# Optimization experiments

Hardware: AMD Instinct MI355X
Metric: run time of the kernel (lower is better)

The kernel has to match this reference:

```python
import jax, jax.numpy as jnp
import numpy as np

START_TIME = 10
CODING_TIME = 10
REMAIN_TIME = 5
V_TH = 1.0

# surrogate-gradient spike: forward is Heaviside(x>0)
@jax.custom_vjp
def spike(x):
    return (x > 0).astype(x.dtype)

def _spike_fwd(x):
    return spike(x), x

def _spike_bwd(x, g):
    lens = 0.5
    gamma = 0.5
    temp = jnp.exp(-x * x / (2.0 * lens * lens)) / jnp.sqrt(2.0 * jnp.pi) / lens
    return (g * temp * gamma,)

spike.defvjp(_spike_fwd, _spike_bwd)

B, T, I, H, O = 500, 100, 700, 512, 20

def setup_inputs() -> dict:
    key = jax.random.key(0)
    ks = jax.random.split(key, 9)
    half = I // 2
    input_data = jax.random.normal(ks[0], (B, T, I), dtype=jnp.float32)
    target = jax.random.randint(ks[1], (B, T), 0, O, dtype=jnp.int32).astype(jnp.int64)
    v_init = jax.random.uniform(ks[2], (B, H), dtype=jnp.float32)  # torch.rand init
    lim = 1.0 / np.sqrt(half)
    W1 = jax.random.uniform(ks[3], (H, half), minval=-lim, maxval=lim, dtype=jnp.float32)
    W2 = jax.random.uniform(ks[4], (H, half), minval=-lim, maxval=lim, dtype=jnp.float32)
    tau_n = jax.random.uniform(ks[5], (2, H), minval=2.0, maxval=6.0, dtype=jnp.float32)
    tau_m = jax.random.uniform(ks[6], (H,), minval=0.0, maxval=4.0, dtype=jnp.float32)
    lim_o = 1.0 / np.sqrt(H)
    Wout = jax.random.uniform(ks[7], (O, H), minval=-lim_o, maxval=lim_o, dtype=jnp.float32)
    bout = jax.random.uniform(ks[8], (O,), minval=-lim_o, maxval=lim_o, dtype=jnp.float32)
    return {"input_data": input_data, "target": target, "v_init": v_init,
            "W1": W1, "W2": W2, "tau_n": tau_n, "tau_m": tau_m,
            "Wout": Wout, "bout": bout}

def reference(input_data, target, v_init, W1, W2, tau_n, tau_m, Wout, bout):
    Bs, Ts, Is = input_data.shape
    half = Is // 2
    # precompute both branch drives for all timesteps: [T, B, H]
    b1 = jnp.einsum('bti,hi->tbh', input_data[:, :, :half], W1)
    b2 = jnp.einsum('bti,hi->tbh', input_data[:, :, half:], W2)
    beta1 = jax.nn.sigmoid(tau_n[0])  # [H]
    beta2 = jax.nn.sigmoid(tau_n[1])  # [H]
    alpha = jax.nn.sigmoid(tau_m)     # [H]

    def step(carry, inp):
        d1, d2, v, s = carry
        x1, x2 = inp
        d1 = beta1 * d1 + (1.0 - beta1) * x1
        d2 = beta2 * d2 + (1.0 - beta2) * x2
        v = alpha * v + (1.0 - alpha) * (d1 + d2) - V_TH * s
        s = spike(v - V_TH)
        return (d1, d2, v, s), s

    z = jnp.zeros_like(v_init)
    (_, _, _, _), spikes = jax.lax.scan(step, (z, z, v_init, z), (b1, b2))  # spikes: [T,B,H]
    output_history = jnp.einsum('tbh,oh->bto', spikes, Wout) + bout  # [B,T,O]

    ts = np.arange(Ts)
    mask_np = ((ts - START_TIME) % (CODING_TIME + REMAIN_TIME) > REMAIN_TIME) & (ts > START_TIME)
    mask = jnp.asarray(mask_np, dtype=output_history.dtype)  # [T]

    # faithful double-softmax: CrossEntropyLoss applied to softmax(output)
    p = jax.nn.softmax(output_history, axis=-1)
    logp = jax.nn.log_softmax(p, axis=-1)
    tgt = target.astype(jnp.int32)
    ce = -jnp.take_along_axis(logp, tgt[..., None], axis=-1)[..., 0]  # [B,T]
    loss_per_t = ce.mean(axis=0)  # mean over batch, per timestep
    total_loss = jnp.sum(loss_per_t * mask)

    pred = jnp.argmax(p, axis=-1)  # [B,T]
    total_correct = jnp.sum((pred == tgt).astype(jnp.int32) * mask_np[None, :].astype(np.int32))
    total_samples = int(mask_np.sum()) * Bs
    return total_loss, output_history, total_correct, total_samples
```

## Files before the change

kernel.cpp:

```cpp
#include <hip/hip_runtime.h>
#include <hip/hip_bf16.h>
#include <math.h>

#define B_    500
#define T_    100
#define I_    700
#define HALF_ 350
#define H_    512
#define O_    20
#define M_    (B_*T_)
#define BH_   (B_*H_)
#define TP_   112
#define KP_   352
#define ASTR_ 40
#define ABUF_ (TP_*ASTR_)
#define DRB_  116
#define NB_   12500

#define START_T  10
#define CODING_T 10
#define REMAIN_T 5

typedef __attribute__((ext_vector_type(8))) short short8v;
typedef __attribute__((ext_vector_type(8))) unsigned short ushort8v;
typedef __attribute__((ext_vector_type(4))) float f32x4;
typedef __attribute__((ext_vector_type(2))) float f32x2;

__device__ __forceinline__ float sigmoidf_(float x) {
  return 1.0f / (1.0f + expf(-x));
}

__device__ __forceinline__ unsigned cvtpk(float lo, float hi) {
  unsigned r;
  asm("v_cvt_pk_bf16_f32 %0, %1, %2" : "=v"(r) : "v"(lo), "v"(hi));
  return r;
}

__device__ __forceinline__ unsigned cvtpk_fp8x4(float f0, float f1, float f2, float f3) {
  int r = __builtin_amdgcn_cvt_pk_fp8_f32(f0, f1, 0, false);
  r = __builtin_amdgcn_cvt_pk_fp8_f32(f2, f3, r, true);
  return (unsigned)r;
}

__device__ __forceinline__ unsigned short f2bf(float f) {
  unsigned u = __float_as_uint(f);
  u = (u + 0x7fffu + ((u >> 16) & 1u)) >> 16;
  return (unsigned short)u;
}

__global__ __launch_bounds__(256) void convert_w(
    const float* __restrict__ W1, const float* __restrict__ W2,
    unsigned short* __restrict__ wb)
{
  const int idx = blockIdx.x * 256 + threadIdx.x;
  const int ph  = idx / (H_ * (KP_ / 8));
  const int rem = idx % (H_ * (KP_ / 8));
  const int h   = rem / (KP_ / 8);
  const int cc  = (rem % (KP_ / 8)) * 8;
  ushort8v v;
#pragma unroll
  for (int j = 0; j < 8; ++j) {
    const int kk = cc + j;
    float f;
    if (ph == 0) f = (kk < HALF_) ? W1[(size_t)h * HALF_ + kk] : 0.0f;
    else         f = (kk >= 2)    ? W2[(size_t)h * HALF_ + kk - 2] : 0.0f;
    v[j] = f2bf(f);
  }
  *reinterpret_cast<ushort8v*>(wb + (((size_t)ph * H_ + h) * KP_) + cc) = v;
}

__global__ __launch_bounds__(1024, 4) void fused_drive_scan(
    const float* __restrict__ input, const unsigned short* __restrict__ Wb,
    const float* __restrict__ v_init, const float* __restrict__ tau_n,
    const float* __restrict__ tau_m, unsigned char* __restrict__ spikes)
{
  __shared__ __align__(16) unsigned short As[2 * ABUF_];
  __shared__ __align__(4) unsigned char d1c[H_ * DRB_];
  __shared__ __align__(4) unsigned char d2c[H_ * DRB_];

  const int tid  = threadIdx.x;
  const int lane = tid & 63;
  const int w    = tid >> 6;
  const int b    = blockIdx.x;

  const int sr = tid >> 3;
  const int so = (tid & 7) * 4;
  const bool stLd = (tid < 800);
  const bool stZr = (tid >= 800) && (tid < 896);
  const float* aBase = input + ((size_t)b * T_ + (stLd ? sr : 0)) * I_ + so;
  unsigned short* aDst = As + sr * ASTR_ + so;

  const int brow = w * 32 + (lane & 15);
  const int kcS  = (lane >> 4) * 8;
  const unsigned short* bBase0 = Wb + (size_t)brow * KP_ + kcS;
  const unsigned short* bBase1 = Wb + (size_t)(brow + 16) * KP_ + kcS;
  const int arow = lane & 15;

  f32x4 acc[7][2];
#pragma unroll
  for (int i = 0; i < 7; ++i) {
    acc[i][0] = f32x4{0.f, 0.f, 0.f, 0.f};
    acc[i][1] = f32x4{0.f, 0.f, 0.f, 0.f};
  }

  float4 aR;
  short8v bC0, bC1, bN0, bN1;

  if (stZr) {
    const uint2 z = {0, 0};
    *(uint2*)(aDst) = z;
    *(uint2*)(aDst + ABUF_) = z;
  }
  if (stLd) aR = *(const float4*)(aBase);
  bC0 = *reinterpret_cast<const short8v*>(bBase0);
  bC1 = *reinterpret_cast<const short8v*>(bBase1);
  bN0 = *reinterpret_cast<const short8v*>(bBase0 + 32);
  bN1 = *reinterpret_cast<const short8v*>(bBase1 + 32);
  if (stLd) {
    const uint2 p = {cvtpk(aR.x, aR.y), cvtpk(aR.z, aR.w)};
    *(uint2*)(aDst) = p;
    aR = *(const float4*)(aBase + 32);
  }
  asm volatile("s_waitcnt lgkmcnt(0)" ::: "memory");
  __builtin_amdgcn_s_barrier();
  asm volatile("" ::: "memory");

#pragma unroll 1
  for (int k = 0; k < 22; ++k) {
    const int buf  = (k & 1) * ABUF_;
    const int nbuf = ((k + 1) & 1) * ABUF_;
    short8v a[7];
#pragma unroll
    for (int i = 0; i < 7; ++i)
      a[i] = *reinterpret_cast<const short8v*>(As + buf + (arow + i * 16) * ASTR_ + kcS);
#pragma unroll
    for (int i = 0; i < 7; ++i) {
      acc[i][0] = __builtin_amdgcn_mfma_f32_16x16x32_bf16(a[i], bC0, acc[i][0], 0, 0, 0);
      acc[i][1] = __builtin_amdgcn_mfma_f32_16x16x32_bf16(a[i], bC1, acc[i][1], 0, 0, 0);
    }
    bC0 = bN0; bC1 = bN1;
    if (k < 21 && stLd) {
      const uint2 p = {cvtpk(aR.x, aR.y), cvtpk(aR.z, aR.w)};
      *(uint2*)(aDst + nbuf) = p;
    }
    if (k < 20 && stLd) {
      const int kn  = k + 2;
      const int ph  = (kn >= 11);
      const int k0  = (kn - ph * 11) * 32;
      aR = *(const float4*)(aBase + (ph ? 348 : 0) + k0);
    }
    if (k < 20) {
      const int kb  = k + 2;
      const int phb = (kb >= 11);
      const size_t bo = (size_t)phb * H_ * KP_ + (kb - phb * 11) * 32;
      bN0 = *reinterpret_cast<const short8v*>(bBase0 + bo);
      bN1 = *reinterpret_cast<const short8v*>(bBase1 + bo);
    }
    if (k == 10 || k == 21) {
      unsigned char* ds = (k == 10) ? d1c : d2c;
#pragma unroll
      for (int i = 0; i < 7; ++i) {
        const int tb = i * 16 + ((lane >> 4) << 2);
#pragma unroll
        for (int j = 0; j < 2; ++j) {
          const int hl = w * 32 + j * 16 + (lane & 15);
          const unsigned r =
              cvtpk_fp8x4(acc[i][j][0], acc[i][j][1], acc[i][j][2], acc[i][j][3]);
          *(unsigned*)(ds + hl * DRB_ + tb) = r;
          acc[i][j] = f32x4{0.f, 0.f, 0.f, 0.f};
        }
      }
    }
    asm volatile("s_waitcnt lgkmcnt(0)" ::: "memory");
    __builtin_amdgcn_s_barrier();
    asm volatile("" ::: "memory");
  }

  if (tid < H_) {
    const int hg = tid;
    const float beta1 = sigmoidf_(tau_n[hg]);
    const float beta2 = sigmoidf_(tau_n[H_ + hg]);
    const float alpha = sigmoidf_(tau_m[hg]);
    const float ob1 = 1.0f - beta1, ob2 = 1.0f - beta2, oa = 1.0f - alpha;

    float d1 = 0.0f, d2 = 0.0f, s = 0.0f;
    float v = v_init[(size_t)b * H_ + hg];
    const unsigned char* r1 = d1c + hg * DRB_;
    const unsigned char* r2 = d2c + hg * DRB_;
    unsigned char* sp = spikes + (size_t)b * H_ + hg;
#pragma unroll 1
    for (int c = 0; c < 25; ++c) {
      const unsigned u1 = *(const unsigned*)(r1 + c * 4);
      const unsigned u2 = *(const unsigned*)(r2 + c * 4);
      const f32x2 a1 = __builtin_amdgcn_cvt_pk_f32_fp8((int)u1, false);
      const f32x2 b1 = __builtin_amdgcn_cvt_pk_f32_fp8((int)u1, true);
      const f32x2 a2 = __builtin_amdgcn_cvt_pk_f32_fp8((int)u2, false);
      const f32x2 b2 = __builtin_amdgcn_cvt_pk_f32_fp8((int)u2, true);
      const float f1[4] = {a1[0], a1[1], b1[0], b1[1]};
      const float f2[4] = {a2[0], a2[1], b2[0], b2[1]};
#pragma unroll
      for (int j = 0; j < 4; ++j) {
        d1 = beta1 * d1 + ob1 * f1[j];
        d2 = beta2 * d2 + ob2 * f2[j];
        v = alpha * v + oa * (d1 + d2) - s;
        s = (v > 1.0f) ? 1.0f : 0.0f;
        sp[(size_t)(c * 4 + j) * BH_] = (unsigned char)s;
      }
    }
  }
}

__global__ __launch_bounds__(256) void out_loss(
    const unsigned char* __restrict__ spikes, const float* __restrict__ Wout,
    const float* __restrict__ bout, const int* __restrict__ target,
    float* __restrict__ oh, float* __restrict__ partials)
{
  const int lane = threadIdx.x & 63;
  const int widx = threadIdx.x >> 6;
  const int bt = blockIdx.x * 4 + widx;
  const int b = bt / T_, t = bt - b * T_;

  const unsigned char* srow = spikes + ((size_t)t * B_ + b) * H_;
  const uint2 sv = *(const uint2*)(srow + lane * 8);

  float acc[O_];
#pragma unroll
  for (int o = 0; o < O_; ++o) acc[o] = 0.0f;

#pragma unroll
  for (int j = 0; j < 8; ++j) {
    const unsigned sb = ((j < 4) ? (sv.x >> (8 * j)) : (sv.y >> (8 * (j - 4)))) & 255u;
    if (sb) {
      const int hh = lane * 8 + j;
#pragma unroll
      for (int o = 0; o < O_; ++o) acc[o] += Wout[o * H_ + hh];
    }
  }
#pragma unroll
  for (int o = 0; o < O_; ++o) {
#pragma unroll
    for (int off = 32; off > 0; off >>= 1) acc[o] += __shfl_down(acc[o], off);
  }

  __shared__ float sl[4], sc[4];
  if (lane == 0) {
    float r[O_];
    float* orow = oh + ((size_t)b * T_ + t) * O_;
#pragma unroll
    for (int o = 0; o < O_; ++o) { r[o] = acc[o] + bout[o]; orow[o] = r[o]; }

    float lossc = 0.0f, corr = 0.0f;
    const bool maskv = (t > START_T) && (((t - START_T) % (CODING_T + REMAIN_T)) > REMAIN_T);
    if (maskv) {
      float m = r[0];
#pragma unroll
      for (int o = 1; o < O_; ++o) m = fmaxf(m, r[o]);
      const int tgt = target[(size_t)b * T_ + t];
      float e[O_], S = 0.0f, etgt = 0.0f;
#pragma unroll
      for (int o = 0; o < O_; ++o) {
        e[o] = expf(r[o] - m);
        S += e[o];
        etgt = (o == tgt) ? e[o] : etgt;
      }
      const float inv = 1.0f / S;
      const float pm = inv;
      float S2 = 0.0f;
#pragma unroll
      for (int o = 0; o < O_; ++o) S2 += expf(e[o] * inv - pm);
      const float lse = pm + logf(S2);
      lossc = (lse - etgt * inv) * (1.0f / (float)B_);
      int pred = 0;
      float bm = r[0];
#pragma unroll
      for (int o = 1; o < O_; ++o) { if (r[o] > bm) { bm = r[o]; pred = o; } }
      corr = (pred == tgt) ? 1.0f : 0.0f;
    }
    sl[widx] = lossc; sc[widx] = corr;
  }
  __syncthreads();
  if (threadIdx.x == 0) {
    partials[blockIdx.x]       = sl[0] + sl[1] + sl[2] + sl[3];
    partials[NB_ + blockIdx.x] = sc[0] + sc[1] + sc[2] + sc[3];
  }
}

__global__ __launch_bounds__(256) void loss_final(
    const float* __restrict__ partials, float* __restrict__ out, float samples)
{
  float a = 0.0f, c = 0.0f;
  for (int i = threadIdx.x; i < NB_; i += 256) { a += partials[i]; c += partials[NB_ + i]; }
  __shared__ float sl[256], sc[256];
  sl[threadIdx.x] = a; sc[threadIdx.x] = c;
  __syncthreads();
  for (int s = 128; s > 0; s >>= 1) {
    if (threadIdx.x < s) {
      sl[threadIdx.x] += sl[threadIdx.x + s];
      sc[threadIdx.x] += sc[threadIdx.x + s];
    }
    __syncthreads();
  }
  if (threadIdx.x == 0) {
    out[0] = sl[0];
    out[1 + (size_t)M_ * O_] = sc[0];
    out[2 + (size_t)M_ * O_] = samples;
  }
}

extern "C" void kernel_launch(void* const* d_in, const int* in_sizes, int n_in,
                              void* d_out, int out_size, void* d_ws, size_t ws_size,
                              hipStream_t stream) {
  const float* input  = (const float*)d_in[0];
  const int*   target = (const int*)d_in[1];
  const float* v_init = (const float*)d_in[2];
  const float* W1     = (const float*)d_in[3];
  const float* W2     = (const float*)d_in[4];
  const float* tau_n  = (const float*)d_in[5];
  const float* tau_m  = (const float*)d_in[6];
  const float* Wout   = (const float*)d_in[7];
  const float* bout   = (const float*)d_in[8];
  float* out = (float*)d_out;
  float* oh  = out + 1;

  unsigned short* Wb = (unsigned short*)d_ws;
  unsigned char* spikes = (unsigned char*)(Wb + (size_t)2 * H_ * KP_);
  float* partials = (float*)(spikes + (size_t)T_ * BH_);

  hipLaunchKernelGGL(convert_w, dim3((2 * H_ * KP_ / 8) / 256), dim3(256), 0, stream,
                     W1, W2, Wb);

  hipLaunchKernelGGL(fused_drive_scan, dim3(B_), dim3(1024), 0, stream,
                     input, Wb, v_init, tau_n, tau_m, spikes);

  hipLaunchKernelGGL(out_loss, dim3(NB_), dim3(256), 0, stream,
                     spikes, Wout, bout, target, oh, partials);

  int mcount = 0;
  for (int t = 0; t < T_; ++t)
    if (t > START_T && ((t - START_T) % (CODING_T + REMAIN_T)) > REMAIN_T) mcount++;
  hipLaunchKernelGGL(loss_final, dim3(1), dim3(256), 0, stream, partials,
                     out, (float)(mcount * B_));
}
```

Measured before the change: 164.9 us.

## Fuse output projection and loss into scan kernel using LDS spike bitmasks

The separate out_loss kernel is removed. Spikes are packed into per-neuron 32-bit bitmasks in shared memory (reusing the A buffer) instead of being written as bytes to global memory. Each of the 16 wavefronts then computes output logits, softmax loss and accuracy for its timesteps and reduces to one partial per batch row. This drops the 25.6 MB spike round trip and a kernel launch. In exchange the scan block does the output work serially per block, and the loss_final reduction shrinks to 500 partials.

```diff
diff --git a/kernel.cpp b/kernel.cpp
--- a/kernel.cpp
+++ b/kernel.cpp
@@ -15,7 +15,6 @@
 #define ASTR_ 40
 #define ABUF_ (TP_*ASTR_)
 #define DRB_  116
-#define NB_   12500
 
 #define START_T  10
 #define CODING_T 10
@@ -69,14 +68,17 @@
   *reinterpret_cast<ushort8v*>(wb + (((size_t)ph * H_ + h) * KP_) + cc) = v;
 }
 
-__global__ __launch_bounds__(1024, 4) void fused_drive_scan(
+__global__ __launch_bounds__(1024, 4) void fused_all(
     const float* __restrict__ input, const unsigned short* __restrict__ Wb,
     const float* __restrict__ v_init, const float* __restrict__ tau_n,
-    const float* __restrict__ tau_m, unsigned char* __restrict__ spikes)
+    const float* __restrict__ tau_m, const float* __restrict__ Wout,
+    const float* __restrict__ bout, const int* __restrict__ target,
+    float* __restrict__ oh, float* __restrict__ partials)
 {
   __shared__ __align__(16) unsigned short As[2 * ABUF_];
   __shared__ __align__(4) unsigned char d1c[H_ * DRB_];
   __shared__ __align__(4) unsigned char d2c[H_ * DRB_];
+  __shared__ float redL[16], redC[16];
 
   const int tid  = threadIdx.x;
   const int lane = tid & 63;
@@ -176,6 +178,7 @@
     asm volatile("" ::: "memory");
   }
 
+  unsigned* sbits = (unsigned*)As;
   if (tid < H_) {
     const int hg = tid;
     const float beta1 = sigmoidf_(tau_n[hg]);
@@ -187,69 +190,76 @@
     float v = v_init[(size_t)b * H_ + hg];
     const unsigned char* r1 = d1c + hg * DRB_;
     const unsigned char* r2 = d2c + hg * DRB_;
-    unsigned char* sp = spikes + (size_t)b * H_ + hg;
+#pragma unroll
+    for (int wi = 0; wi < 4; ++wi) {
+      unsigned bits = 0;
+#pragma unroll
+      for (int cc = 0; cc < 8; ++cc) {
+        if (wi == 3 && cc >= 1) break;
+        const int c = wi * 8 + cc;
+        const unsigned u1 = *(const unsigned*)(r1 + c * 4);
+        const unsigned u2 = *(const unsigned*)(r2 + c * 4);
+        const f32x2 a1 = __builtin_amdgcn_cvt_pk_f32_fp8((int)u1, false);
+        const f32x2 b1 = __builtin_amdgcn_cvt_pk_f32_fp8((int)u1, true);
+        const f32x2 a2 = __builtin_amdgcn_cvt_pk_f32_fp8((int)u2, false);
+        const f32x2 b2 = __builtin_amdgcn_cvt_pk_f32_fp8((int)u2, true);
+        const float f1[4] = {a1[0], a1[1], b1[0], b1[1]};
+        const float f2[4] = {a2[0], a2[1], b2[0], b2[1]};
+#pragma unroll
+        for (int j = 0; j < 4; ++j) {
+          d1 = beta1 * d1 + ob1 * f1[j];
+          d2 = beta2 * d2 + ob2 * f2[j];
+          v = alpha * v + oa * (d1 + d2) - s;
+          const bool spk = (v > 1.0f);
+          s = spk ? 1.0f : 0.0f;
+          bits |= ((unsigned)spk) << (cc * 4 + j);
+        }
+      }
+      sbits[wi * H_ + hg] = bits;
+    }
+  }
+  __syncthreads();
+
+  float bo[O_];
+#pragma unroll
+  for (int o = 0; o < O_; ++o) bo[o] = bout[o];
+
+  float lossAcc = 0.0f, corrAcc = 0.0f;
+  const int hbase = lane * 8;
 #pragma unroll 1
-    for (int c = 0; c < 25; ++c) {
-      const unsigned u1 = *(const unsigned*)(r1 + c * 4);
-      const unsigned u2 = *(const unsigned*)(r2 + c * 4);
-      const f32x2 a1 = __builtin_amdgcn_cvt_pk_f32_fp8((int)u1, false);
-      const f32x2 b1 = __builtin_amdgcn_cvt_pk_f32_fp8((int)u1, true);
-      const f32x2 a2 = __builtin_amdgcn_cvt_pk_f32_fp8((int)u2, false);
-      const f32x2 b2 = __builtin_amdgcn_cvt_pk_f32_fp8((int)u2, true);
-      const float f1[4] = {a1[0], a1[1], b1[0], b1[1]};
-      const float f2[4] = {a2[0], a2[1], b2[0], b2[1]};
-#pragma unroll
-      for (int j = 0; j < 4; ++j) {
-        d1 = beta1 * d1 + ob1 * f1[j];
-        d2 = beta2 * d2 + ob2 * f2[j];
-        v = alpha * v + oa * (d1 + d2) - s;
-        s = (v > 1.0f) ? 1.0f : 0.0f;
-        sp[(size_t)(c * 4 + j) * BH_] = (unsigned char)s;
+  for (int t = w; t < T_; t += 16) {
+    const unsigned* sb = sbits + (t >> 5) * H_ + hbase;
+    const uint4 wa = *(const uint4*)(sb);
+    const uint4 wb2 = *(const uint4*)(sb + 4);
+    const unsigned sel = t & 31;
+    const unsigned wv[8] = {wa.x, wa.y, wa.z, wa.w, wb2.x, wb2.y, wb2.z, wb2.w};
+
+    float acco[O_];
+#pragma unroll
+    for (int o = 0; o < O_; ++o) acco[o] = 0.0f;
+#pragma unroll
+    for (int j = 0; j < 8; ++j) {
+      if ((wv[j] >> sel) & 1u) {
+        const int hh = hbase + j;
+#pragma unroll
+        for (int o = 0; o < O_; ++o) acco[o] += Wout[o * H_ + hh];
       }
     }
-  }
-}
-
-__global__ __launch_bounds__(256) void out_loss(
-    const unsigned char* __restrict__ spikes, const float* __restrict__ Wout,
-    const float* __restrict__ bout, const int* __restrict__ target,
-    float* __restrict__ oh, float* __restrict__ partials)
-{
-  const int lane = threadIdx.x & 63;
-  const int widx = threadIdx.x >> 6;
-  const int bt = blockIdx.x * 4 + widx;
-  const int b = bt / T_, t = bt - b * T_;
-
-  const unsigned char* srow = spikes + ((size_t)t * B_ + b) * H_;
-  const uint2 sv = *(const uint2*)(srow + lane * 8);
-
-  float acc[O_];
-#pragma unroll
-  for (int o = 0; o < O_; ++o) acc[o] = 0.0f;
-
-#pragma unroll
-  for (int j = 0; j < 8; ++j) {
-    const unsigned sb = ((j < 4) ? (sv.x >> (8 * j)) : (sv.y >> (8 * (j - 4)))) & 255u;
-    if (sb) {
-      const int hh = lane * 8 + j;
-#pragma unroll
-      for (int o = 0; o < O_; ++o) acc[o] += Wout[o * H_ + hh];
-    }
-  }
-#pragma unroll
-  for (int o = 0; o < O_; ++o) {
-#pragma unroll
-    for (int off = 32; off > 0; off >>= 1) acc[o] += __shfl_down(acc[o], off);
-  }
-
-  __shared__ float sl[4], sc[4];
-  if (lane == 0) {
+#pragma unroll
+    for (int o = 0; o < O_; ++o) {
+#pragma unroll
+      for (int off = 32; off; off >>= 1) acco[o] += __shfl_xor(acco[o], off);
+    }
     float r[O_];
-    float* orow = oh + ((size_t)b * T_ + t) * O_;
-#pragma unroll
-    for (int o = 0; o < O_; ++o) { r[o] = acc[o] + bout[o]; orow[o] = r[o]; }
-
-    float lossc = 0.0f, corr = 0.0f;
+#pragma unroll
+    for (int o = 0; o < O_; ++o) r[o] = acco[o] + bo[o];
+
+    if (lane == 0) {
+      float* orow = oh + ((size_t)b * T_ + t) * O_;
+#pragma unroll
+      for (int o = 0; o < O_; ++o) orow[o] = r[o];
+    }
+
     const bool maskv = (t > START_T) && (((t - START_T) % (CODING_T + REMAIN_T)) > REMAIN_T);
     if (maskv) {
       float m = r[0];
@@ -269,19 +279,22 @@
 #pragma unroll
       for (int o = 0; o < O_; ++o) S2 += expf(e[o] * inv - pm);
       const float lse = pm + logf(S2);
-      lossc = (lse - etgt * inv) * (1.0f / (float)B_);
+      lossAcc += (lse - etgt * inv) * (1.0f / (float)B_);
       int pred = 0;
       float bm = r[0];
 #pragma unroll
       for (int o = 1; o < O_; ++o) { if (r[o] > bm) { bm = r[o]; pred = o; } }
-      corr = (pred == tgt) ? 1.0f : 0.0f;
-    }
-    sl[widx] = lossc; sc[widx] = corr;
-  }
+      corrAcc += (pred == tgt) ? 1.0f : 0.0f;
+    }
+  }
+  if (lane == 0) { redL[w] = lossAcc; redC[w] = corrAcc; }
   __syncthreads();
-  if (threadIdx.x == 0) {
-    partials[blockIdx.x]       = sl[0] + sl[1] + sl[2] + sl[3];
-    partials[NB_ + blockIdx.x] = sc[0] + sc[1] + sc[2] + sc[3];
+  if (tid == 0) {
+    float L = 0.0f, C = 0.0f;
+#pragma unroll
+    for (int i = 0; i < 16; ++i) { L += redL[i]; C += redC[i]; }
+    partials[b] = L;
+    partials[B_ + b] = C;
   }
 }
 
@@ -289,7 +302,7 @@
     const float* __restrict__ partials, float* __restrict__ out, float samples)
 {
   float a = 0.0f, c = 0.0f;
-  for (int i = threadIdx.x; i < NB_; i += 256) { a += partials[i]; c += partials[NB_ + i]; }
+  for (int i = threadIdx.x; i < B_; i += 256) { a += partials[i]; c += partials[B_ + i]; }
   __shared__ float sl[256], sc[256];
   sl[threadIdx.x] = a; sc[threadIdx.x] = c;
   __syncthreads();
@@ -323,17 +336,14 @@
   float* oh  = out + 1;
 
   unsigned short* Wb = (unsigned short*)d_ws;
-  unsigned char* spikes = (unsigned char*)(Wb + (size_t)2 * H_ * KP_);
-  float* partials = (float*)(spikes + (size_t)T_ * BH_);
+  float* partials = (float*)(Wb + (size_t)2 * H_ * KP_);
 
   hipLaunchKernelGGL(convert_w, dim3((2 * H_ * KP_ / 8) / 256), dim3(256), 0, stream,
                      W1, W2, Wb);
 
-  hipLaunchKernelGGL(fused_drive_scan, dim3(B_), dim3(1024), 0, stream,
-                     input, Wb, v_init, tau_n, tau_m, spikes);
-
-  hipLaunchKernelGGL(out_loss, dim3(NB_), dim3(256), 0, stream,
-                     spikes, Wout, bout, target, oh, partials);
+  hipLaunchKernelGGL(fused_all, dim3(B_), dim3(1024), 0, stream,
+                     input, Wb, v_init, tau_n, tau_m, Wout, bout, target,
+                     oh, partials);
 
   int mcount = 0;
   for (int t = 0; t < T_; ++t)
```

New measurement: 350.7 us. 2.13x slower.

## Store spikes batch-major and process one batch per out_loss block

Applied to the files above, without the earlier changes.

The scan kernel now writes spikes in [B,T,H] order instead of [T,B,H], so each batch's spike history is contiguous. out_loss launches one block per batch (500 instead of 12500), stages that batch's 51 KB spike tile into LDS, and loops each wave over timesteps while accumulating loss and correctness locally. This cuts the number of partials and the final reduction work, but the loop over timesteps is serial per block and the grid has far fewer blocks, which may reduce parallelism. The exp is recomputed in the second softmax pass instead of being stored in an array.

```diff
diff --git a/kernel.cpp b/kernel.cpp
--- a/kernel.cpp
+++ b/kernel.cpp
@@ -15,7 +15,6 @@
 #define ASTR_ 40
 #define ABUF_ (TP_*ASTR_)
 #define DRB_  116
-#define NB_   12500
 
 #define START_T  10
 #define CODING_T 10
@@ -187,7 +186,7 @@
     float v = v_init[(size_t)b * H_ + hg];
     const unsigned char* r1 = d1c + hg * DRB_;
     const unsigned char* r2 = d2c + hg * DRB_;
-    unsigned char* sp = spikes + (size_t)b * H_ + hg;
+    unsigned char* sp = spikes + (size_t)b * (T_ * H_) + hg;
 #pragma unroll 1
     for (int c = 0; c < 25; ++c) {
       const unsigned u1 = *(const unsigned*)(r1 + c * 4);
@@ -204,7 +203,7 @@
         d2 = beta2 * d2 + ob2 * f2[j];
         v = alpha * v + oa * (d1 + d2) - s;
         s = (v > 1.0f) ? 1.0f : 0.0f;
-        sp[(size_t)(c * 4 + j) * BH_] = (unsigned char)s;
+        sp[(size_t)(c * 4 + j) * H_] = (unsigned char)s;
       }
     }
   }
@@ -215,73 +214,76 @@
     const float* __restrict__ bout, const int* __restrict__ target,
     float* __restrict__ oh, float* __restrict__ partials)
 {
-  const int lane = threadIdx.x & 63;
-  const int widx = threadIdx.x >> 6;
-  const int bt = blockIdx.x * 4 + widx;
-  const int b = bt / T_, t = bt - b * T_;
-
-  const unsigned char* srow = spikes + ((size_t)t * B_ + b) * H_;
-  const uint2 sv = *(const uint2*)(srow + lane * 8);
-
-  float acc[O_];
-#pragma unroll
-  for (int o = 0; o < O_; ++o) acc[o] = 0.0f;
-
-#pragma unroll
-  for (int j = 0; j < 8; ++j) {
-    const unsigned sb = ((j < 4) ? (sv.x >> (8 * j)) : (sv.y >> (8 * (j - 4)))) & 255u;
-    if (sb) {
-      const int hh = lane * 8 + j;
-#pragma unroll
-      for (int o = 0; o < O_; ++o) acc[o] += Wout[o * H_ + hh];
-    }
-  }
-#pragma unroll
-  for (int o = 0; o < O_; ++o) {
-#pragma unroll
-    for (int off = 32; off > 0; off >>= 1) acc[o] += __shfl_down(acc[o], off);
-  }
-
-  __shared__ float sl[4], sc[4];
-  if (lane == 0) {
-    float r[O_];
-    float* orow = oh + ((size_t)b * T_ + t) * O_;
-#pragma unroll
-    for (int o = 0; o < O_; ++o) { r[o] = acc[o] + bout[o]; orow[o] = r[o]; }
-
-    float lossc = 0.0f, corr = 0.0f;
+  __shared__ __align__(16) unsigned char sp_lds[T_ * H_];
+  __shared__ float redL[4], redC[4];
+
+  const int tid  = threadIdx.x;
+  const int lane = tid & 63;
+  const int w    = tid >> 6;
+  const int b    = blockIdx.x;
+
+  {
+    const uint4* src = (const uint4*)(spikes + (size_t)b * (T_ * H_));
+    uint4* dst = (uint4*)sp_lds;
+#pragma unroll 1
+    for (int i = tid; i < (T_ * H_) / 16; i += 256) dst[i] = src[i];
+  }
+  __syncthreads();
+
+  float lossAcc = 0.0f, corrAcc = 0.0f;
+#pragma unroll 1
+  for (int t = w; t < T_; t += 4) {
+    const uint2 sv = *(const uint2*)(sp_lds + t * H_ + lane * 8);
+    float acc[O_];
+#pragma unroll
+    for (int o = 0; o < O_; ++o) acc[o] = 0.0f;
+#pragma unroll
+    for (int j = 0; j < 8; ++j) {
+      const unsigned sb = ((j < 4) ? (sv.x >> (8 * j)) : (sv.y >> (8 * (j - 4)))) & 255u;
+      if (sb) {
+        const int hh = lane * 8 + j;
+#pragma unroll
+        for (int o = 0; o < O_; ++o) acc[o] += Wout[o * H_ + hh];
+      }
+    }
+#pragma unroll
+    for (int o = 0; o < O_; ++o) {
+#pragma unroll
+      for (int off = 32; off; off >>= 1) acc[o] += __shfl_xor(acc[o], off);
+      acc[o] += bout[o];
+    }
+    if (lane == 0) {
+      float* orow = oh + ((size_t)b * T_ + t) * O_;
+#pragma unroll
+      for (int o = 0; o < O_; ++o) orow[o] = acc[o];
+    }
     const bool maskv = (t > START_T) && (((t - START_T) % (CODING_T + REMAIN_T)) > REMAIN_T);
     if (maskv) {
-      float m = r[0];
-#pragma unroll
-      for (int o = 1; o < O_; ++o) m = fmaxf(m, r[o]);
       const int tgt = target[(size_t)b * T_ + t];
-      float e[O_], S = 0.0f, etgt = 0.0f;
+      float m = acc[0];
+      int pred = 0;
+#pragma unroll
+      for (int o = 1; o < O_; ++o) { if (acc[o] > m) { m = acc[o]; pred = o; } }
+      float S = 0.0f, etgt = 0.0f;
 #pragma unroll
       for (int o = 0; o < O_; ++o) {
-        e[o] = expf(r[o] - m);
-        S += e[o];
-        etgt = (o == tgt) ? e[o] : etgt;
+        const float eo = expf(acc[o] - m);
+        S += eo;
+        if (o == tgt) etgt = eo;
       }
       const float inv = 1.0f / S;
-      const float pm = inv;
       float S2 = 0.0f;
 #pragma unroll
-      for (int o = 0; o < O_; ++o) S2 += expf(e[o] * inv - pm);
-      const float lse = pm + logf(S2);
-      lossc = (lse - etgt * inv) * (1.0f / (float)B_);
-      int pred = 0;
-      float bm = r[0];
-#pragma unroll
-      for (int o = 1; o < O_; ++o) { if (r[o] > bm) { bm = r[o]; pred = o; } }
-      corr = (pred == tgt) ? 1.0f : 0.0f;
-    }
-    sl[widx] = lossc; sc[widx] = corr;
-  }
+      for (int o = 0; o < O_; ++o) S2 += expf(expf(acc[o] - m) * inv - inv);
+      lossAcc += (inv + logf(S2) - etgt * inv) * (1.0f / (float)B_);
+      corrAcc += (pred == tgt) ? 1.0f : 0.0f;
+    }
+  }
+  if (lane == 0) { redL[w] = lossAcc; redC[w] = corrAcc; }
   __syncthreads();
-  if (threadIdx.x == 0) {
-    partials[blockIdx.x]       = sl[0] + sl[1] + sl[2] + sl[3];
-    partials[NB_ + blockIdx.x] = sc[0] + sc[1] + sc[2] + sc[3];
+  if (tid == 0) {
+    partials[b]      = redL[0] + redL[1] + redL[2] + redL[3];
+    partials[B_ + b] = redC[0] + redC[1] + redC[2] + redC[3];
   }
 }
 
@@ -289,7 +291,7 @@
     const float* __restrict__ partials, float* __restrict__ out, float samples)
 {
   float a = 0.0f, c = 0.0f;
-  for (int i = threadIdx.x; i < NB_; i += 256) { a += partials[i]; c += partials[NB_ + i]; }
+  for (int i = threadIdx.x; i < B_; i += 256) { a += partials[i]; c += partials[B_ + i]; }
   __shared__ float sl[256], sc[256];
   sl[threadIdx.x] = a; sc[threadIdx.x] = c;
   __syncthreads();
@@ -324,7 +326,7 @@
 
   unsigned short* Wb = (unsigned short*)d_ws;
   unsigned char* spikes = (unsigned char*)(Wb + (size_t)2 * H_ * KP_);
-  float* partials = (float*)(spikes + (size_t)T_ * BH_);
+  float* partials = (float*)(spikes + (size_t)B_ * T_ * H_);
 
   hipLaunchKernelGGL(convert_w, dim3((2 * H_ * KP_ / 8) / 256), dim3(256), 0, stream,
                      W1, W2, Wb);
@@ -332,7 +334,7 @@
   hipLaunchKernelGGL(fused_drive_scan, dim3(B_), dim3(1024), 0, stream,
                      input, Wb, v_init, tau_n, tau_m, spikes);
 
-  hipLaunchKernelGGL(out_loss, dim3(NB_), dim3(256), 0, stream,
+  hipLaunchKernelGGL(out_loss, dim3(B_), dim3(256), 0, stream,
                      spikes, Wout, bout, target, oh, partials);
 
   int mcount = 0;
```

Measured after the change: 256.6 us. 55.5% more time.
